# Optimization experiments

Hardware: AMD Instinct MI355X
Metric: run time of the kernel (lower is better)

The kernel has to match this reference:

```python
import jax, jax.numpy as jnp
import numpy as np

B, I, H, O = 65536, 128, 256, 256

def setup_inputs() -> dict:
    key = jax.random.key(0)
    ks = jax.random.split(key, 6)
    s_h = 1.0 / np.sqrt(I + H)
    return {
        "input": jax.random.normal(ks[0], (B, I), jnp.float32),
        "hidden": jax.random.normal(ks[1], (B, H), jnp.float32),
        "w_i2h": jax.random.uniform(ks[2], (4 * H, I + H), jnp.float32, -s_h, s_h),
        "b_i2h": jax.random.uniform(ks[3], (4 * H,), jnp.float32, -s_h, s_h),
        "w_i2o": jax.random.uniform(ks[4], (O, I + H), jnp.float32, -s_h, s_h),
        "b_i2o": jax.random.uniform(ks[5], (O,), jnp.float32, -s_h, s_h),
    }

def reference(input, hidden, w_i2h, b_i2h, w_i2o, b_i2o):
    # combined: [B, I+H]
    combined = jnp.concatenate([input, hidden], axis=1)
    gates = combined @ w_i2h.T + b_i2h            # [B, 4H]
    h, ig, fg, og = jnp.split(gates, 4, axis=1)   # each [B, H]
    ig = jax.nn.sigmoid(ig)
    fg = jax.nn.sigmoid(fg)
    og = jax.nn.sigmoid(og)
    h = jnp.tanh(h)
    new_hidden = og * jnp.tanh(fg * hidden + ig * h)
    output = jax.nn.log_softmax(combined @ w_i2o.T + b_i2o, axis=1)  # [B, O]
    return (output, new_hidden)
```

## Files before the change

### kernel.cpp

```cpp
#include <hip/hip_runtime.h>
#include <hip/hip_bf16.h>
#include <math.h>


typedef __attribute__((ext_vector_type(8))) short bf16x8;
typedef __attribute__((ext_vector_type(4))) float f32x4;

#define BM   64
#define LDA  392
#define NW1  393216
#define NW2  98304

__device__ __forceinline__ unsigned short f2bf(float f) {
    union { __hip_bfloat16 h; unsigned short u; } cv;
    cv.h = __float2bfloat16(f);
    return cv.u;
}
__device__ __forceinline__ float bf2f(unsigned short u) {
    union { __hip_bfloat16 h; unsigned short u; } cv;
    cv.u = u;
    return __bfloat162float(cv.h);
}
__device__ __forceinline__ float frcp(float x) {
    return __builtin_amdgcn_rcpf(x);
}
__device__ __forceinline__ float fsigmoid(float x) {
    return frcp(1.0f + __expf(-x));
}
__device__ __forceinline__ float ftanh(float x) {
    return 1.0f - 2.0f * frcp(__expf(2.0f * x) + 1.0f);
}

__global__ void conv_w(const float* __restrict__ w1, const float* __restrict__ w2,
                       unsigned short* __restrict__ wb) {
    int idx = blockIdx.x * 256 + threadIdx.x;
    const int n1 = NW1 / 4;
    float4 v;
    if (idx < n1) v = ((const float4*)w1)[idx];
    else          v = ((const float4*)w2)[idx - n1];
    ushort4 u;
    u.x = f2bf(v.x); u.y = f2bf(v.y); u.z = f2bf(v.z); u.w = f2bf(v.w);
    ((ushort4*)wb)[idx] = u;
}

__launch_bounds__(256, 2)
__global__ void lstm_fused(const float* __restrict__ input,
                           const float* __restrict__ hidden,
                           const unsigned short* __restrict__ w1b,
                           const unsigned short* __restrict__ w2b,
                           const float* __restrict__ b1,
                           const float* __restrict__ b2,
                           float* __restrict__ out_ls,
                           float* __restrict__ out_nh)
{
    __shared__ unsigned short A[BM * LDA];
    __shared__ float red_m[4][BM];
    __shared__ float red_s[4][BM];

    const int tid  = threadIdx.x;
    const int wave = tid >> 6;
    const int lane = tid & 63;
    const int l15  = lane & 15;
    const int quad = lane >> 4;
    const size_t r0 = (size_t)blockIdx.x * BM;

    {
        const int row = tid >> 2;
        const int c0  = tid & 3;
        const float4* si = (const float4*)(input  + (r0 + row) * 128);
        const float4* sh = (const float4*)(hidden + (r0 + row) * 256);
        ushort4* dst = (ushort4*)&A[row * LDA];
        #pragma unroll
        for (int i = 0; i < 24; ++i) {
            int c4 = c0 + 4 * i;
            float4 v = (i < 8) ? si[c4] : sh[c4 - 32];
            union { __hip_bfloat162 h2; unsigned int u; } p0, p1;
            p0.h2 = __float22bfloat162_rn(make_float2(v.x, v.y));
            p1.h2 = __float22bfloat162_rn(make_float2(v.z, v.w));
            union { ushort4 s4; uint2 u2; } st;
            st.u2 = make_uint2(p0.u, p1.u);
            dst[c4] = st.s4;
        }
    }
    __syncthreads();

    const unsigned short* ap0 = &A[l15 * LDA + quad * 8];

    const unsigned short* bp[4];
    {
        int j0 = 0 * 64 + wave * 16;
        #pragma unroll
        for (int q = 0; q < 4; ++q)
            bp[q] = w1b + (size_t)(q * 256 + j0 + l15) * 384 + quad * 8;
    }

    bf16x8 acur[4], bcur[4];
    #pragma unroll
    for (int mt = 0; mt < 4; ++mt)
        acur[mt] = *(const bf16x8*)(ap0 + mt * 16 * LDA);
    #pragma unroll
    for (int nt = 0; nt < 4; ++nt)
        bcur[nt] = *(const bf16x8*)(bp[nt]);

    #pragma unroll 1
    for (int phase = 0; phase < 5; ++phase) {
        const int j = phase * 64 + wave * 16 + l15;
        unsigned short hp[16];
        float bq0, bq1, bq2, bq3;
        float bo[4];
        if (phase < 4) {
            #pragma unroll
            for (int mt = 0; mt < 4; ++mt)
                #pragma unroll
                for (int r = 0; r < 4; ++r)
                    hp[mt * 4 + r] = A[(mt * 16 + quad * 4 + r) * LDA + 128 + j];
            bq0 = b1[j]; bq1 = b1[256 + j]; bq2 = b1[512 + j]; bq3 = b1[768 + j];
        } else {
            #pragma unroll
            for (int nt = 0; nt < 4; ++nt) bo[nt] = b2[wave * 64 + nt * 16 + l15];
        }

        f32x4 acc[4][4];
        #pragma unroll
        for (int i = 0; i < 4; ++i)
            #pragma unroll
            for (int jj = 0; jj < 4; ++jj)
                acc[i][jj] = (f32x4){0.f, 0.f, 0.f, 0.f};

        #pragma unroll
        for (int kk = 0; kk < 12; ++kk) {
            bf16x8 anxt[4], bnxt[4];
            if (kk < 11) {
                #pragma unroll
                for (int mt = 0; mt < 4; ++mt)
                    anxt[mt] = *(const bf16x8*)(ap0 + mt * 16 * LDA + (kk + 1) * 32);
                #pragma unroll
                for (int nt = 0; nt < 4; ++nt)
                    bnxt[nt] = *(const bf16x8*)(bp[nt] + (kk + 1) * 32);
            } else {
                int pn = phase + 1;
                if (pn < 4) {
                    int j0 = pn * 64 + wave * 16;
                    #pragma unroll
                    for (int q = 0; q < 4; ++q)
                        bp[q] = w1b + (size_t)(q * 256 + j0 + l15) * 384 + quad * 8;
                } else {
                    #pragma unroll
                    for (int nt = 0; nt < 4; ++nt)
                        bp[nt] = w2b + (size_t)(wave * 64 + nt * 16 + l15) * 384 + quad * 8;
                }
                #pragma unroll
                for (int mt = 0; mt < 4; ++mt)
                    anxt[mt] = *(const bf16x8*)(ap0 + mt * 16 * LDA);
                #pragma unroll
                for (int nt = 0; nt < 4; ++nt)
                    bnxt[nt] = *(const bf16x8*)(bp[nt]);
            }
            #pragma unroll
            for (int mt = 0; mt < 4; ++mt)
                #pragma unroll
                for (int nt = 0; nt < 4; ++nt)
                    acc[mt][nt] = __builtin_amdgcn_mfma_f32_16x16x32_bf16(
                        acur[mt], bcur[nt], acc[mt][nt], 0, 0, 0);
            #pragma unroll
            for (int mt = 0; mt < 4; ++mt) acur[mt] = anxt[mt];
            #pragma unroll
            for (int nt = 0; nt < 4; ++nt) bcur[nt] = bnxt[nt];
        }

        if (phase < 4) {
            #pragma unroll
            for (int mt = 0; mt < 4; ++mt) {
                #pragma unroll
                for (int r = 0; r < 4; ++r) {
                    int rowl = mt * 16 + quad * 4 + r;
                    float hprev = bf2f(hp[mt * 4 + r]);
                    float hv  = ftanh(acc[mt][0][r] + bq0);
                    float igv = fsigmoid(acc[mt][1][r] + bq1);
                    float fgv = fsigmoid(acc[mt][2][r] + bq2);
                    float ogv = fsigmoid(acc[mt][3][r] + bq3);
                    out_nh[(r0 + rowl) * 256 + j] = ogv * ftanh(fgv * hprev + igv * hv);
                }
            }
        } else {
            #pragma unroll
            for (int mt = 0; mt < 4; ++mt)
                #pragma unroll
                for (int nt = 0; nt < 4; ++nt)
                    #pragma unroll
                    for (int r = 0; r < 4; ++r)
                        acc[mt][nt][r] += bo[nt];

            float pm[4][4], ps[4][4];
            #pragma unroll
            for (int mt = 0; mt < 4; ++mt)
                #pragma unroll
                for (int r = 0; r < 4; ++r) {
                    float m = acc[mt][0][r];
                    #pragma unroll
                    for (int nt = 1; nt < 4; ++nt) m = fmaxf(m, acc[mt][nt][r]);
                    pm[mt][r] = m;
                }
            #pragma unroll
            for (int mask = 1; mask < 16; mask <<= 1)
                #pragma unroll
                for (int mt = 0; mt < 4; ++mt)
                    #pragma unroll
                    for (int r = 0; r < 4; ++r)
                        pm[mt][r] = fmaxf(pm[mt][r], __shfl_xor(pm[mt][r], mask, 64));
            #pragma unroll
            for (int mt = 0; mt < 4; ++mt)
                #pragma unroll
                for (int r = 0; r < 4; ++r) {
                    float s = 0.f;
                    #pragma unroll
                    for (int nt = 0; nt < 4; ++nt)
                        s += __expf(acc[mt][nt][r] - pm[mt][r]);
                    ps[mt][r] = s;
                }
            #pragma unroll
            for (int mask = 1; mask < 16; mask <<= 1)
                #pragma unroll
                for (int mt = 0; mt < 4; ++mt)
                    #pragma unroll
                    for (int r = 0; r < 4; ++r)
                        ps[mt][r] += __shfl_xor(ps[mt][r], mask, 64);

            if (l15 == 0) {
                #pragma unroll
                for (int mt = 0; mt < 4; ++mt)
                    #pragma unroll
                    for (int r = 0; r < 4; ++r) {
                        int rowl = mt * 16 + quad * 4 + r;
                        red_m[wave][rowl] = pm[mt][r];
                        red_s[wave][rowl] = ps[mt][r];
                    }
            }
            __syncthreads();
            #pragma unroll
            for (int mt = 0; mt < 4; ++mt)
                #pragma unroll
                for (int r = 0; r < 4; ++r) {
                    int rowl = mt * 16 + quad * 4 + r;
                    float M = red_m[0][rowl];
                    #pragma unroll
                    for (int w = 1; w < 4; ++w) M = fmaxf(M, red_m[w][rowl]);
                    float S = 0.f;
                    #pragma unroll
                    for (int w = 0; w < 4; ++w)
                        S += red_s[w][rowl] * __expf(red_m[w][rowl] - M);
                    float lz = M + 0.69314718055994531f * __log2f(S);
                    #pragma unroll
                    for (int nt = 0; nt < 4; ++nt)
                        out_ls[(r0 + rowl) * 256 + wave * 64 + nt * 16 + l15] =
                            acc[mt][nt][r] - lz;
                }
        }
    }
}

extern "C" void kernel_launch(void* const* d_in, const int* in_sizes, int n_in,
                              void* d_out, int out_size, void* d_ws, size_t ws_size,
                              hipStream_t stream) {
    const float* input  = (const float*)d_in[0];
    const float* hidden = (const float*)d_in[1];
    const float* w1     = (const float*)d_in[2];
    const float* b1     = (const float*)d_in[3];
    const float* w2     = (const float*)d_in[4];
    const float* b2     = (const float*)d_in[5];
    float* out = (float*)d_out;
    unsigned short* wb = (unsigned short*)d_ws;

    conv_w<<<dim3((NW1 + NW2) / 4 / 256), dim3(256), 0, stream>>>(w1, w2, wb);
    lstm_fused<<<dim3(65536 / BM), dim3(256), 0, stream>>>(
        input, hidden, wb, wb + NW1, b1, b2,
        out, out + (size_t)65536 * 256);
}
```

Before: 333.8 us.

## Split block into 8 waves with 2x4 tile grid and triple-buffered weight prefetch

Doubles the block to 512 threads, arranged as two row groups of four waves, so each wave computes a 32x64 tile instead of 64x64. This halves per-wave accumulator registers and targets higher occupancy, which helps hide global weight-load latency. The B-fragment prefetch becomes a 3-stage register ring that loads two k-steps ahead, and the first weight loads are issued before the activation staging. The cost is more waves loading the same weight fragments per block, and therefore more redundant global/L2 weight traffic.

```diff
diff --git a/kernel.cpp b/kernel.cpp
--- a/kernel.cpp
+++ b/kernel.cpp
@@ -43,7 +43,7 @@
     ((ushort4*)wb)[idx] = u;
 }
 
-__launch_bounds__(256, 2)
+__launch_bounds__(512, 4)
 __global__ void lstm_fused(const float* __restrict__ input,
                            const float* __restrict__ hidden,
                            const unsigned short* __restrict__ w1b,
@@ -62,18 +62,30 @@
     const int lane = tid & 63;
     const int l15  = lane & 15;
     const int quad = lane >> 4;
+    const int wg   = wave >> 2;
+    const int wc   = wave & 3;
     const size_t r0 = (size_t)blockIdx.x * BM;
 
+    const unsigned short* bp[4];
+    #pragma unroll
+    for (int q = 0; q < 4; ++q)
+        bp[q] = w1b + (size_t)(q * 256 + wc * 16 + l15) * 384 + quad * 8;
+    bf16x8 bfr[3][4];
+    #pragma unroll
+    for (int nt = 0; nt < 4; ++nt) bfr[0][nt] = *(const bf16x8*)(bp[nt]);
+    #pragma unroll
+    for (int nt = 0; nt < 4; ++nt) bfr[1][nt] = *(const bf16x8*)(bp[nt] + 32);
+
     {
-        const int row = tid >> 2;
-        const int c0  = tid & 3;
+        const int row = tid >> 3;
+        const int c0  = tid & 7;
         const float4* si = (const float4*)(input  + (r0 + row) * 128);
         const float4* sh = (const float4*)(hidden + (r0 + row) * 256);
         ushort4* dst = (ushort4*)&A[row * LDA];
         #pragma unroll
-        for (int i = 0; i < 24; ++i) {
-            int c4 = c0 + 4 * i;
-            float4 v = (i < 8) ? si[c4] : sh[c4 - 32];
+        for (int i = 0; i < 12; ++i) {
+            int c4 = c0 + 8 * i;
+            float4 v = (i < 4) ? si[c4] : sh[c4 - 32];
             union { __hip_bfloat162 h2; unsigned int u; } p0, p1;
             p0.h2 = __float22bfloat162_rn(make_float2(v.x, v.y));
             p1.h2 = __float22bfloat162_rn(make_float2(v.z, v.w));
@@ -84,96 +96,96 @@
     }
     __syncthreads();
 
-    const unsigned short* ap0 = &A[l15 * LDA + quad * 8];
-
-    const unsigned short* bp[4];
-    {
-        int j0 = 0 * 64 + wave * 16;
-        #pragma unroll
-        for (int q = 0; q < 4; ++q)
-            bp[q] = w1b + (size_t)(q * 256 + j0 + l15) * 384 + quad * 8;
-    }
-
-    bf16x8 acur[4], bcur[4];
-    #pragma unroll
-    for (int mt = 0; mt < 4; ++mt)
-        acur[mt] = *(const bf16x8*)(ap0 + mt * 16 * LDA);
-    #pragma unroll
-    for (int nt = 0; nt < 4; ++nt)
-        bcur[nt] = *(const bf16x8*)(bp[nt]);
+    const unsigned short* ap0 = &A[(wg * 32 + l15) * LDA + quad * 8];
+    bf16x8 afr[2][2];
+    #pragma unroll
+    for (int mt = 0; mt < 2; ++mt)
+        afr[0][mt] = *(const bf16x8*)(ap0 + mt * 16 * LDA);
 
     #pragma unroll 1
     for (int phase = 0; phase < 5; ++phase) {
-        const int j = phase * 64 + wave * 16 + l15;
-        unsigned short hp[16];
+        const int j = phase * 64 + wc * 16 + l15;
+        unsigned short hp[8];
         float bq0, bq1, bq2, bq3;
         float bo[4];
         if (phase < 4) {
             #pragma unroll
-            for (int mt = 0; mt < 4; ++mt)
+            for (int mt = 0; mt < 2; ++mt)
                 #pragma unroll
                 for (int r = 0; r < 4; ++r)
-                    hp[mt * 4 + r] = A[(mt * 16 + quad * 4 + r) * LDA + 128 + j];
+                    hp[mt * 4 + r] = A[(wg * 32 + mt * 16 + quad * 4 + r) * LDA + 128 + j];
             bq0 = b1[j]; bq1 = b1[256 + j]; bq2 = b1[512 + j]; bq3 = b1[768 + j];
         } else {
             #pragma unroll
-            for (int nt = 0; nt < 4; ++nt) bo[nt] = b2[wave * 64 + nt * 16 + l15];
-        }
-
-        f32x4 acc[4][4];
+            for (int nt = 0; nt < 4; ++nt) bo[nt] = b2[wc * 64 + nt * 16 + l15];
+        }
+
+        f32x4 acc[2][4];
         #pragma unroll
-        for (int i = 0; i < 4; ++i)
+        for (int i = 0; i < 2; ++i)
             #pragma unroll
             for (int jj = 0; jj < 4; ++jj)
                 acc[i][jj] = (f32x4){0.f, 0.f, 0.f, 0.f};
 
         #pragma unroll
         for (int kk = 0; kk < 12; ++kk) {
-            bf16x8 anxt[4], bnxt[4];
-            if (kk < 11) {
-                #pragma unroll
-                for (int mt = 0; mt < 4; ++mt)
-                    anxt[mt] = *(const bf16x8*)(ap0 + mt * 16 * LDA + (kk + 1) * 32);
+            const int cs  = kk % 3;
+            const int ns  = (kk + 2) % 3;
+            const int as_ = kk & 1;
+            const int an  = (kk + 1) & 1;
+
+            if (kk < 10) {
                 #pragma unroll
                 for (int nt = 0; nt < 4; ++nt)
-                    bnxt[nt] = *(const bf16x8*)(bp[nt] + (kk + 1) * 32);
-            } else {
+                    bfr[ns][nt] = *(const bf16x8*)(bp[nt] + (kk + 2) * 32);
+            } else if (kk == 10) {
                 int pn = phase + 1;
                 if (pn < 4) {
-                    int j0 = pn * 64 + wave * 16;
                     #pragma unroll
                     for (int q = 0; q < 4; ++q)
-                        bp[q] = w1b + (size_t)(q * 256 + j0 + l15) * 384 + quad * 8;
-                } else {
-                    #pragma unroll
-                    for (int nt = 0; nt < 4; ++nt)
-                        bp[nt] = w2b + (size_t)(wave * 64 + nt * 16 + l15) * 384 + quad * 8;
-                }
-                #pragma unroll
-                for (int mt = 0; mt < 4; ++mt)
-                    anxt[mt] = *(const bf16x8*)(ap0 + mt * 16 * LDA);
-                #pragma unroll
-                for (int nt = 0; nt < 4; ++nt)
-                    bnxt[nt] = *(const bf16x8*)(bp[nt]);
-            }
-            #pragma unroll
-            for (int mt = 0; mt < 4; ++mt)
+                        bp[q] = w1b + (size_t)(q * 256 + pn * 64 + wc * 16 + l15) * 384 + quad * 8;
+                    #pragma unroll
+                    for (int nt = 0; nt < 4; ++nt)
+                        bfr[0][nt] = *(const bf16x8*)(bp[nt]);
+                } else if (pn == 4) {
+                    #pragma unroll
+                    for (int nt = 0; nt < 4; ++nt)
+                        bp[nt] = w2b + (size_t)(wc * 64 + nt * 16 + l15) * 384 + quad * 8;
+                    #pragma unroll
+                    for (int nt = 0; nt < 4; ++nt)
+                        bfr[0][nt] = *(const bf16x8*)(bp[nt]);
+                }
+            } else {
+                if (phase < 4) {
+                    #pragma unroll
+                    for (int nt = 0; nt < 4; ++nt)
+                        bfr[1][nt] = *(const bf16x8*)(bp[nt] + 32);
+                }
+            }
+            if (kk < 11) {
+                #pragma unroll
+                for (int mt = 0; mt < 2; ++mt)
+                    afr[an][mt] = *(const bf16x8*)(ap0 + mt * 16 * LDA + (kk + 1) * 32);
+            } else {
+                #pragma unroll
+                for (int mt = 0; mt < 2; ++mt)
+                    afr[0][mt] = *(const bf16x8*)(ap0 + mt * 16 * LDA);
+            }
+
+            #pragma unroll
+            for (int mt = 0; mt < 2; ++mt)
                 #pragma unroll
                 for (int nt = 0; nt < 4; ++nt)
                     acc[mt][nt] = __builtin_amdgcn_mfma_f32_16x16x32_bf16(
-                        acur[mt], bcur[nt], acc[mt][nt], 0, 0, 0);
-            #pragma unroll
-            for (int mt = 0; mt < 4; ++mt) acur[mt] = anxt[mt];
-            #pragma unroll
-            for (int nt = 0; nt < 4; ++nt) bcur[nt] = bnxt[nt];
+                        afr[as_][mt], bfr[cs][nt], acc[mt][nt], 0, 0, 0);
         }
 
         if (phase < 4) {
             #pragma unroll
-            for (int mt = 0; mt < 4; ++mt) {
-                #pragma unroll
-                for (int r = 0; r < 4; ++r) {
-                    int rowl = mt * 16 + quad * 4 + r;
+            for (int mt = 0; mt < 2; ++mt) {
+                #pragma unroll
+                for (int r = 0; r < 4; ++r) {
+                    int rowl = wg * 32 + mt * 16 + quad * 4 + r;
                     float hprev = bf2f(hp[mt * 4 + r]);
                     float hv  = ftanh(acc[mt][0][r] + bq0);
                     float igv = fsigmoid(acc[mt][1][r] + bq1);
@@ -184,16 +196,16 @@
             }
         } else {
             #pragma unroll
-            for (int mt = 0; mt < 4; ++mt)
+            for (int mt = 0; mt < 2; ++mt)
                 #pragma unroll
                 for (int nt = 0; nt < 4; ++nt)
                     #pragma unroll
                     for (int r = 0; r < 4; ++r)
                         acc[mt][nt][r] += bo[nt];
 
-            float pm[4][4], ps[4][4];
-            #pragma unroll
-            for (int mt = 0; mt < 4; ++mt)
+            float pm[2][4], ps[2][4];
+            #pragma unroll
+            for (int mt = 0; mt < 2; ++mt)
                 #pragma unroll
                 for (int r = 0; r < 4; ++r) {
                     float m = acc[mt][0][r];
@@ -204,12 +216,12 @@
             #pragma unroll
             for (int mask = 1; mask < 16; mask <<= 1)
                 #pragma unroll
-                for (int mt = 0; mt < 4; ++mt)
+                for (int mt = 0; mt < 2; ++mt)
                     #pragma unroll
                     for (int r = 0; r < 4; ++r)
                         pm[mt][r] = fmaxf(pm[mt][r], __shfl_xor(pm[mt][r], mask, 64));
             #pragma unroll
-            for (int mt = 0; mt < 4; ++mt)
+            for (int mt = 0; mt < 2; ++mt)
                 #pragma unroll
                 for (int r = 0; r < 4; ++r) {
                     float s = 0.f;
@@ -221,27 +233,27 @@
             #pragma unroll
             for (int mask = 1; mask < 16; mask <<= 1)
                 #pragma unroll
-                for (int mt = 0; mt < 4; ++mt)
+                for (int mt = 0; mt < 2; ++mt)
                     #pragma unroll
                     for (int r = 0; r < 4; ++r)
                         ps[mt][r] += __shfl_xor(ps[mt][r], mask, 64);
 
             if (l15 == 0) {
                 #pragma unroll
-                for (int mt = 0; mt < 4; ++mt)
+                for (int mt = 0; mt < 2; ++mt)
                     #pragma unroll
                     for (int r = 0; r < 4; ++r) {
-                        int rowl = mt * 16 + quad * 4 + r;
-                        red_m[wave][rowl] = pm[mt][r];
-                        red_s[wave][rowl] = ps[mt][r];
+                        int rowl = wg * 32 + mt * 16 + quad * 4 + r;
+                        red_m[wc][rowl] = pm[mt][r];
+                        red_s[wc][rowl] = ps[mt][r];
                     }
             }
             __syncthreads();
             #pragma unroll
-            for (int mt = 0; mt < 4; ++mt)
-                #pragma unroll
-                for (int r = 0; r < 4; ++r) {
-                    int rowl = mt * 16 + quad * 4 + r;
+            for (int mt = 0; mt < 2; ++mt)
+                #pragma unroll
+                for (int r = 0; r < 4; ++r) {
+                    int rowl = wg * 32 + mt * 16 + quad * 4 + r;
                     float M = red_m[0][rowl];
                     #pragma unroll
                     for (int w = 1; w < 4; ++w) M = fmaxf(M, red_m[w][rowl]);
@@ -252,7 +264,7 @@
                     float lz = M + 0.69314718055994531f * __log2f(S);
                     #pragma unroll
                     for (int nt = 0; nt < 4; ++nt)
-                        out_ls[(r0 + rowl) * 256 + wave * 64 + nt * 16 + l15] =
+                        out_ls[(r0 + rowl) * 256 + wc * 64 + nt * 16 + l15] =
                             acc[mt][nt][r] - lz;
                 }
         }
@@ -272,7 +284,7 @@
     unsigned short* wb = (unsigned short*)d_ws;
 
     conv_w<<<dim3((NW1 + NW2) / 4 / 256), dim3(256), 0, stream>>>(w1, w2, wb);
-    lstm_fused<<<dim3(65536 / BM), dim3(256), 0, stream>>>(
+    lstm_fused<<<dim3(65536 / BM), dim3(512), 0, stream>>>(
         input, hidden, wb, wb + NW1, b1, b2,
         out, out + (size_t)65536 * 256);
 }
```

Measured after the change: 439.6 us. 1.32x slower.

## Triple-buffer weight fragments with prefetch distance two and raise occupancy

Applied to the files above, without the earlier changes.

Weight (B) fragments are now prefetched two K-steps ahead into a three-slot register ring. The first fetches are issued before the activation tile is staged into shared memory, so global latency overlaps the staging work. Activation (A) fragments are read from shared memory just in time instead of being double-buffered in registers, which frees registers. The launch bound moves from 2 to 3 blocks per CU to hide latency with more waves. The risk is register spills or LDS limits under the higher occupancy, since three 50KB tiles nearly fill shared memory.

```diff
diff --git a/kernel.cpp b/kernel.cpp
--- a/kernel.cpp
+++ b/kernel.cpp
@@ -43,7 +43,7 @@
     ((ushort4*)wb)[idx] = u;
 }
 
-__launch_bounds__(256, 2)
+__launch_bounds__(256, 3)
 __global__ void lstm_fused(const float* __restrict__ input,
                            const float* __restrict__ hidden,
                            const unsigned short* __restrict__ w1b,
@@ -63,6 +63,16 @@
     const int l15  = lane & 15;
     const int quad = lane >> 4;
     const size_t r0 = (size_t)blockIdx.x * BM;
+
+    const unsigned short* bp[4];
+    #pragma unroll
+    for (int q = 0; q < 4; ++q)
+        bp[q] = w1b + (size_t)(q * 256 + wave * 16 + l15) * 384 + quad * 8;
+    bf16x8 bfr[3][4];
+    #pragma unroll
+    for (int nt = 0; nt < 4; ++nt) bfr[0][nt] = *(const bf16x8*)(bp[nt]);
+    #pragma unroll
+    for (int nt = 0; nt < 4; ++nt) bfr[1][nt] = *(const bf16x8*)(bp[nt] + 32);
 
     {
         const int row = tid >> 2;
@@ -86,22 +96,6 @@
 
     const unsigned short* ap0 = &A[l15 * LDA + quad * 8];
 
-    const unsigned short* bp[4];
-    {
-        int j0 = 0 * 64 + wave * 16;
-        #pragma unroll
-        for (int q = 0; q < 4; ++q)
-            bp[q] = w1b + (size_t)(q * 256 + j0 + l15) * 384 + quad * 8;
-    }
-
-    bf16x8 acur[4], bcur[4];
-    #pragma unroll
-    for (int mt = 0; mt < 4; ++mt)
-        acur[mt] = *(const bf16x8*)(ap0 + mt * 16 * LDA);
-    #pragma unroll
-    for (int nt = 0; nt < 4; ++nt)
-        bcur[nt] = *(const bf16x8*)(bp[nt]);
-
     #pragma unroll 1
     for (int phase = 0; phase < 5; ++phase) {
         const int j = phase * 64 + wave * 16 + l15;
@@ -129,43 +123,44 @@
 
         #pragma unroll
         for (int kk = 0; kk < 12; ++kk) {
-            bf16x8 anxt[4], bnxt[4];
-            if (kk < 11) {
-                #pragma unroll
-                for (int mt = 0; mt < 4; ++mt)
-                    anxt[mt] = *(const bf16x8*)(ap0 + mt * 16 * LDA + (kk + 1) * 32);
+            if (kk < 10) {
                 #pragma unroll
                 for (int nt = 0; nt < 4; ++nt)
-                    bnxt[nt] = *(const bf16x8*)(bp[nt] + (kk + 1) * 32);
-            } else {
+                    bfr[(kk + 2) % 3][nt] = *(const bf16x8*)(bp[nt] + (kk + 2) * 32);
+            } else if (kk == 10) {
                 int pn = phase + 1;
                 if (pn < 4) {
-                    int j0 = pn * 64 + wave * 16;
                     #pragma unroll
                     for (int q = 0; q < 4; ++q)
-                        bp[q] = w1b + (size_t)(q * 256 + j0 + l15) * 384 + quad * 8;
-                } else {
+                        bp[q] = w1b + (size_t)(q * 256 + pn * 64 + wave * 16 + l15) * 384 + quad * 8;
+                    #pragma unroll
+                    for (int nt = 0; nt < 4; ++nt)
+                        bfr[0][nt] = *(const bf16x8*)(bp[nt]);
+                } else if (pn == 4) {
                     #pragma unroll
                     for (int nt = 0; nt < 4; ++nt)
                         bp[nt] = w2b + (size_t)(wave * 64 + nt * 16 + l15) * 384 + quad * 8;
-                }
-                #pragma unroll
-                for (int mt = 0; mt < 4; ++mt)
-                    anxt[mt] = *(const bf16x8*)(ap0 + mt * 16 * LDA);
-                #pragma unroll
-                for (int nt = 0; nt < 4; ++nt)
-                    bnxt[nt] = *(const bf16x8*)(bp[nt]);
+                    #pragma unroll
+                    for (int nt = 0; nt < 4; ++nt)
+                        bfr[0][nt] = *(const bf16x8*)(bp[nt]);
+                }
+            } else {
+                if (phase < 4) {
+                    #pragma unroll
+                    for (int nt = 0; nt < 4; ++nt)
+                        bfr[1][nt] = *(const bf16x8*)(bp[nt] + 32);
+                }
             }
+            bf16x8 a[4];
+            #pragma unroll
+            for (int mt = 0; mt < 4; ++mt)
+                a[mt] = *(const bf16x8*)(ap0 + mt * 16 * LDA + kk * 32);
             #pragma unroll
             for (int mt = 0; mt < 4; ++mt)
                 #pragma unroll
                 for (int nt = 0; nt < 4; ++nt)
                     acc[mt][nt] = __builtin_amdgcn_mfma_f32_16x16x32_bf16(
-                        acur[mt], bcur[nt], acc[mt][nt], 0, 0, 0);
-            #pragma unroll
-            for (int mt = 0; mt < 4; ++mt) acur[mt] = anxt[mt];
-            #pragma unroll
-            for (int nt = 0; nt < 4; ++nt) bcur[nt] = bnxt[nt];
+                        a[mt], bfr[kk % 3][nt], acc[mt][nt], 0, 0, 0);
         }
 
         if (phase < 4) {
```

After: 408.8 us. 22.4% more time.
